# Kernel tuning notes

Hardware: AMD Instinct MI355X
Metric: run time of the kernel (lower is better)

Reference implementation:

```python
import jax, jax.numpy as jnp
import numpy as np

N_NODES = 50000
N_EDGES = 800000
D_IN = 128
D_HID = 128
D_OUT = 128


def setup_inputs() -> dict:
    key = jax.random.key(0)
    ks = jax.random.split(key, 10)
    x = jax.random.normal(ks[0], (N_NODES, D_IN), dtype=jnp.float32)
    edge_index = jax.random.randint(ks[1], (2, N_EDGES), 0, N_NODES, dtype=jnp.int64)
    edge_index_inter = jax.random.randint(ks[2], (2, N_EDGES), 0, N_NODES, dtype=jnp.int64)
    # nn.Linear-style params: W [out, in], b [out]
    def linear(k, fan_in, fan_out):
        k1, k2 = jax.random.split(k)
        bound = 1.0 / np.sqrt(fan_in)
        W = jax.random.uniform(k1, (fan_out, fan_in), minval=-bound, maxval=bound, dtype=jnp.float32)
        b = jax.random.uniform(k2, (fan_out,), minval=-bound, maxval=bound, dtype=jnp.float32)
        return W, b
    W1, b1 = linear(ks[3], D_IN, D_HID)
    W2, b2 = linear(ks[4], D_HID, D_HID)
    W3, b3 = linear(ks[5], D_HID, D_OUT)
    return {"x": x, "W1": W1, "b1": b1, "W2": W2, "b2": b2, "W3": W3, "b3": b3,
            "edge_index": edge_index, "edge_index_inter": edge_index_inter}


def _gnn_layer(h, W, b, src, dst, n_nodes):
    # message: lin(x_j - x_i); x_j = source features, x_i = target features (PyG convention)
    msg = (h[src] - h[dst]) @ W.T + b          # [E, out]
    # aggr='add': scatter-add messages into target nodes
    return jax.ops.segment_sum(msg, dst, num_segments=n_nodes)  # [N, out]


def reference(x, W1, b1, W2, b2, W3, b3, edge_index, edge_index_inter):
    src, dst = edge_index[0], edge_index[1]
    n = x.shape[0]
    h = _gnn_layer(x, W1, b1, src, dst, n)
    h = _gnn_layer(h, W2, b2, src, dst, n)
    return _gnn_layer(h, W3, b3, src, dst, n)
```

## Files before the change

### kernel.cpp

```cpp
#include <hip/hip_runtime.h>

#define N_NODES 50000
#define N_EDGES 800000
#define D 128
#define TN 16
#define TSTR 136
#define SCAN_BLOCKS 196

typedef __attribute__((ext_vector_type(8))) short bf16x8;
typedef __attribute__((ext_vector_type(4))) float f32x4;

__device__ __forceinline__ unsigned short f32_to_bf16_rne(float f) {
    unsigned u = __float_as_uint(f);
    u += 0x7fffu + ((u >> 16) & 1u);
    return (unsigned short)(u >> 16);
}

__global__ void prep_kernel(const int* __restrict__ dst, int* __restrict__ counts,
                            const float* __restrict__ x, unsigned short* __restrict__ xb) {
    const int t = blockIdx.x * blockDim.x + threadIdx.x;
    if (t < N_EDGES) atomicAdd(&counts[dst[t]], 1);
    {
        const float4 v0 = *(const float4*)(x + (size_t)t * 8);
        const float4 v1 = *(const float4*)(x + (size_t)t * 8 + 4);
        uint4 p;
        p.x = (unsigned)f32_to_bf16_rne(v0.x) | ((unsigned)f32_to_bf16_rne(v0.y) << 16);
        p.y = (unsigned)f32_to_bf16_rne(v0.z) | ((unsigned)f32_to_bf16_rne(v0.w) << 16);
        p.z = (unsigned)f32_to_bf16_rne(v1.x) | ((unsigned)f32_to_bf16_rne(v1.y) << 16);
        p.w = (unsigned)f32_to_bf16_rne(v1.z) | ((unsigned)f32_to_bf16_rne(v1.w) << 16);
        *(uint4*)(xb + (size_t)t * 8) = p;
    }
}

__global__ void block_sum_kernel(const int* __restrict__ counts, int* __restrict__ bsum) {
    __shared__ int red[256];
    const int tid = threadIdx.x;
    const int i = blockIdx.x * 256 + tid;
    red[tid] = (i < N_NODES) ? counts[i] : 0;
    __syncthreads();
    for (int s = 128; s > 0; s >>= 1) {
        if (tid < s) red[tid] += red[tid + s];
        __syncthreads();
    }
    if (tid == 0) bsum[blockIdx.x] = red[0];
}

__global__ void bsum_scan_kernel(const int* __restrict__ bsum,
                                 int* __restrict__ bpre,
                                 int* __restrict__ offsets) {
    __shared__ int s[256];
    const int tid = threadIdx.x;
    const int v = (tid < SCAN_BLOCKS) ? bsum[tid] : 0;
    s[tid] = v;
    __syncthreads();
    for (int off = 1; off < 256; off <<= 1) {
        int a = (tid >= off) ? s[tid - off] : 0;
        __syncthreads();
        s[tid] += a;
        __syncthreads();
    }
    bpre[tid] = s[tid] - v;
    if (tid == 255) offsets[N_NODES] = s[255];
}

__global__ void offsets_wfrag_kernel(const int* __restrict__ counts,
                                     const int* __restrict__ bpre,
                                     int* __restrict__ offsets,
                                     int* __restrict__ cursor,
                                     const float* __restrict__ W1,
                                     const float* __restrict__ W2,
                                     const float* __restrict__ W3,
                                     unsigned short* __restrict__ Wb) {
    if (blockIdx.x < SCAN_BLOCKS) {
        __shared__ int s[256];
        const int tid = threadIdx.x;
        const int i = blockIdx.x * 256 + tid;
        const int v = (i < N_NODES) ? counts[i] : 0;
        s[tid] = v;
        __syncthreads();
        for (int off = 1; off < 256; off <<= 1) {
            int a = (tid >= off) ? s[tid - off] : 0;
            __syncthreads();
            s[tid] += a;
            __syncthreads();
        }
        const int excl = s[tid] - v + bpre[blockIdx.x];
        if (i < N_NODES) {
            offsets[i] = excl;
            cursor[i] = excl;
        }
    } else {
        const int unit = (blockIdx.x - SCAN_BLOCKS) * 2 + (threadIdx.x >> 7);
        const int w = unit >> 7;
        const int o = unit & 127;
        const int k = threadIdx.x & 127;
        const float* W = (w == 0) ? W1 : (w == 1) ? W2 : W3;
        const unsigned short v = f32_to_bf16_rne(W[o * D + k]);
        const int nt = o >> 4, n = o & 15;
        const int kc = k >> 5, kr = k & 31, quad = kr >> 3, j = kr & 7;
        const int lane = quad * 16 + n;
        Wb[(((size_t)w * 8 + nt) * 4 + kc) * 512 + lane * 8 + j] = v;
    }
}

__global__ void fill_kernel(const int* __restrict__ src, const int* __restrict__ dst,
                            int* __restrict__ cursor, int* __restrict__ esrc) {
    int e = blockIdx.x * blockDim.x + threadIdx.x;
    if (e < N_EDGES) {
        int v = dst[e];
        int p = atomicAdd(&cursor[v], 1);
        esrc[p] = src[e];
    }
}

template <bool OUT_BF16>
__global__ __launch_bounds__(256) void gnn_layer_kernel(
    const unsigned short* __restrict__ hb,
    const int* __restrict__ offsets,
    const int* __restrict__ esrc,
    const unsigned short* __restrict__ Wb,
    const float* __restrict__ bias,
    float* __restrict__ outf,
    unsigned short* __restrict__ outb) {

    __shared__ __align__(16) unsigned short tb[TN][TSTR];
    __shared__ float degf[TN];

    const int tid = threadIdx.x;
    const int wave = tid >> 6;
    const int lane = tid & 63;
    const int sub = lane >> 5;
    const int q = lane & 31;
    const int vbase = blockIdx.x * TN;

    for (int j = wave * 4; j < wave * 4 + 4; ++j) {
        const int v = vbase + j;
        const int beg = offsets[v];
        const int end = offsets[v + 1];
        const int deg = end - beg;

        float a0x = 0.f, a0y = 0.f, a0z = 0.f, a0w = 0.f;
        float a1x = 0.f, a1y = 0.f, a1z = 0.f, a1w = 0.f;
        float a2x = 0.f, a2y = 0.f, a2z = 0.f, a2w = 0.f;
        float a3x = 0.f, a3y = 0.f, a3z = 0.f, a3w = 0.f;

        if (deg <= 64) {
            int myidx = 0;
            if (lane < deg) myidx = esrc[beg + lane];

            int i = 0;
            for (; i + 8 <= deg; i += 8) {
                const int s0 = __shfl(myidx, i + sub, 64);
                const int s1 = __shfl(myidx, i + 2 + sub, 64);
                const int s2 = __shfl(myidx, i + 4 + sub, 64);
                const int s3 = __shfl(myidx, i + 6 + sub, 64);
                const uint2 r0 = *(const uint2*)(hb + (size_t)s0 * D + 4 * q);
                const uint2 r1 = *(const uint2*)(hb + (size_t)s1 * D + 4 * q);
                const uint2 r2 = *(const uint2*)(hb + (size_t)s2 * D + 4 * q);
                const uint2 r3 = *(const uint2*)(hb + (size_t)s3 * D + 4 * q);
                a0x += __uint_as_float(r0.x << 16); a0y += __uint_as_float(r0.x & 0xffff0000u);
                a0z += __uint_as_float(r0.y << 16); a0w += __uint_as_float(r0.y & 0xffff0000u);
                a1x += __uint_as_float(r1.x << 16); a1y += __uint_as_float(r1.x & 0xffff0000u);
                a1z += __uint_as_float(r1.y << 16); a1w += __uint_as_float(r1.y & 0xffff0000u);
                a2x += __uint_as_float(r2.x << 16); a2y += __uint_as_float(r2.x & 0xffff0000u);
                a2z += __uint_as_float(r2.y << 16); a2w += __uint_as_float(r2.y & 0xffff0000u);
                a3x += __uint_as_float(r3.x << 16); a3y += __uint_as_float(r3.x & 0xffff0000u);
                a3z += __uint_as_float(r3.y << 16); a3w += __uint_as_float(r3.y & 0xffff0000u);
            }
            for (; i + 2 <= deg; i += 2) {
                const int s0 = __shfl(myidx, i + sub, 64);
                const uint2 r0 = *(const uint2*)(hb + (size_t)s0 * D + 4 * q);
                a0x += __uint_as_float(r0.x << 16); a0y += __uint_as_float(r0.x & 0xffff0000u);
                a0z += __uint_as_float(r0.y << 16); a0w += __uint_as_float(r0.y & 0xffff0000u);
            }
            if (i < deg) {
                const int s0 = __shfl(myidx, i, 64);
                if (sub == 0) {
                    const uint2 r0 = *(const uint2*)(hb + (size_t)s0 * D + 4 * q);
                    a0x += __uint_as_float(r0.x << 16); a0y += __uint_as_float(r0.x & 0xffff0000u);
                    a0z += __uint_as_float(r0.y << 16); a0w += __uint_as_float(r0.y & 0xffff0000u);
                }
            }
        } else {
            for (int e = beg; e < end; e += 2) {
                const int e0 = e + sub;
                if (e0 < end) {
                    const uint2 r0 = *(const uint2*)(hb + (size_t)esrc[e0] * D + 4 * q);
                    a0x += __uint_as_float(r0.x << 16); a0y += __uint_as_float(r0.x & 0xffff0000u);
                    a0z += __uint_as_float(r0.y << 16); a0w += __uint_as_float(r0.y & 0xffff0000u);
                }
            }
        }

        float ax = (a0x + a1x) + (a2x + a3x);
        float ay = (a0y + a1y) + (a2y + a3y);
        float az = (a0z + a1z) + (a2z + a3z);
        float aw = (a0w + a1w) + (a2w + a3w);

        ax += __shfl_xor(ax, 32, 64);
        ay += __shfl_xor(ay, 32, 64);
        az += __shfl_xor(az, 32, 64);
        aw += __shfl_xor(aw, 32, 64);

        const float dv = (float)deg;
        if (sub == 0) {
            const uint2 r = *(const uint2*)(hb + (size_t)v * D + 4 * q);
            const float tx = ax - dv * __uint_as_float(r.x << 16);
            const float ty = ay - dv * __uint_as_float(r.x & 0xffff0000u);
            const float tz = az - dv * __uint_as_float(r.y << 16);
            const float tw = aw - dv * __uint_as_float(r.y & 0xffff0000u);
            unsigned p0 = (unsigned)f32_to_bf16_rne(tx) | ((unsigned)f32_to_bf16_rne(ty) << 16);
            unsigned p1 = (unsigned)f32_to_bf16_rne(tz) | ((unsigned)f32_to_bf16_rne(tw) << 16);
            *(uint2*)&tb[j][4 * q] = make_uint2(p0, p1);
        }
        if (lane == 0) degf[j] = dv;
    }
    __syncthreads();

    const int n16 = lane & 15;
    const int quad = lane >> 4;

    bf16x8 afrag[4];
#pragma unroll
    for (int kc = 0; kc < 4; ++kc)
        afrag[kc] = *(const bf16x8*)&tb[n16][kc * 32 + quad * 8];

#pragma unroll
    for (int i = 0; i < 2; ++i) {
        const int nt = wave * 2 + i;
        f32x4 acc = {0.f, 0.f, 0.f, 0.f};
#pragma unroll
        for (int kc = 0; kc < 4; ++kc) {
            const bf16x8 bfrag = *(const bf16x8*)&Wb[((nt * 4 + kc) * 64 + lane) * 8];
            acc = __builtin_amdgcn_mfma_f32_16x16x32_bf16(afrag[kc], bfrag, acc, 0, 0, 0);
        }
        const int o = nt * 16 + n16;
        const float bo = bias[o];
#pragma unroll
        for (int r = 0; r < 4; ++r) {
            const int m = quad * 4 + r;
            const float val = acc[r] + degf[m] * bo;
            if (OUT_BF16)
                outb[(size_t)(vbase + m) * D + o] = f32_to_bf16_rne(val);
            else
                outf[(size_t)(vbase + m) * D + o] = val;
        }
    }
}

extern "C" void kernel_launch(void* const* d_in, const int* in_sizes, int n_in,
                              void* d_out, int out_size, void* d_ws, size_t ws_size,
                              hipStream_t stream) {
    const float* x  = (const float*)d_in[0];
    const float* W1 = (const float*)d_in[1];
    const float* b1 = (const float*)d_in[2];
    const float* W2 = (const float*)d_in[3];
    const float* b2 = (const float*)d_in[4];
    const float* W3 = (const float*)d_in[5];
    const float* b3 = (const float*)d_in[6];
    const int*   ei = (const int*)d_in[7];

    const int* src = ei;
    const int* dst = ei + N_EDGES;
    float* out = (float*)d_out;

    char* ws = (char*)d_ws;
    int* counts  = (int*)ws;                      ws += 204800;
    int* offsets = (int*)ws;                      ws += 204800;
    int* cursor  = (int*)ws;                      ws += 204800;
    int* bsum    = (int*)ws;                      ws += 1024;
    int* bpre    = (int*)ws;                      ws += 1024;
    int* esrc    = (int*)ws;                      ws += (size_t)N_EDGES * 4;
    unsigned short* Wb = (unsigned short*)ws;     ws += 3 * 16384 * 2;
    unsigned short* xb = (unsigned short*)ws;     ws += (size_t)N_NODES * D * 2;
    unsigned short* h1 = (unsigned short*)ws;     ws += (size_t)N_NODES * D * 2;
    unsigned short* h2 = (unsigned short*)ws;

    hipMemsetAsync(counts, 0, N_NODES * sizeof(int), stream);
    prep_kernel<<<(N_EDGES + 255) / 256, 256, 0, stream>>>(dst, counts, x, xb);
    block_sum_kernel<<<SCAN_BLOCKS, 256, 0, stream>>>(counts, bsum);
    bsum_scan_kernel<<<1, 256, 0, stream>>>(bsum, bpre, offsets);
    offsets_wfrag_kernel<<<SCAN_BLOCKS + 192, 256, 0, stream>>>(counts, bpre, offsets, cursor,
                                                                W1, W2, W3, Wb);
    fill_kernel<<<(N_EDGES + 255) / 256, 256, 0, stream>>>(src, dst, cursor, esrc);

    const int blocks = N_NODES / TN;

    gnn_layer_kernel<true ><<<blocks, 256, 0, stream>>>(xb, offsets, esrc, Wb,          b1, nullptr, h1);
    gnn_layer_kernel<true ><<<blocks, 256, 0, stream>>>(h1, offsets, esrc, Wb + 16384,  b2, nullptr, h2);
    gnn_layer_kernel<false><<<blocks, 256, 0, stream>>>(h2, offsets, esrc, Wb + 32768,  b3, out, nullptr);
}
```

Before: 289.4 us.

## Split fused gather+GEMM into separate column-sliced gather and MFMA GEMM kernels

Splits each layer's fused aggregate-then-MFMA kernel into two kernels. The first is a gather that splits the 128 features into four 32-column slices, one per block group, with a wave per node and 8 edges processed in parallel per pass. The second is a small GEMM kernel that reads the aggregated bf16 rows from a global buffer. CSR construction also records per-edge atomic ranks during counting, which removes the second atomic cursor pass in fill. The cost is an extra global round-trip of the aggregated tensor and more kernel launches, in exchange for finer-grained gather parallelism and a possibly better cache footprint per feature slice.

```diff
diff --git a/kernel.cpp b/kernel.cpp
--- a/kernel.cpp
+++ b/kernel.cpp
@@ -3,7 +3,6 @@
 #define N_NODES 50000
 #define N_EDGES 800000
 #define D 128
-#define TN 16
 #define TSTR 136
 #define SCAN_BLOCKS 196
 
@@ -16,10 +15,20 @@
     return (unsigned short)(u >> 16);
 }
 
+__device__ __forceinline__ void acc_bf16x4(uint2 r, float& x, float& y, float& z, float& w) {
+    x += __uint_as_float(r.x << 16);
+    y += __uint_as_float(r.x & 0xffff0000u);
+    z += __uint_as_float(r.y << 16);
+    w += __uint_as_float(r.y & 0xffff0000u);
+}
+
 __global__ void prep_kernel(const int* __restrict__ dst, int* __restrict__ counts,
+                            int* __restrict__ rank,
                             const float* __restrict__ x, unsigned short* __restrict__ xb) {
     const int t = blockIdx.x * blockDim.x + threadIdx.x;
-    if (t < N_EDGES) atomicAdd(&counts[dst[t]], 1);
+    if (t < N_EDGES) {
+        rank[t] = atomicAdd(&counts[dst[t]], 1);
+    }
     {
         const float4 v0 = *(const float4*)(x + (size_t)t * 8);
         const float4 v1 = *(const float4*)(x + (size_t)t * 8 + 4);
@@ -66,7 +75,6 @@
 __global__ void offsets_wfrag_kernel(const int* __restrict__ counts,
                                      const int* __restrict__ bpre,
                                      int* __restrict__ offsets,
-                                     int* __restrict__ cursor,
                                      const float* __restrict__ W1,
                                      const float* __restrict__ W2,
                                      const float* __restrict__ W3,
@@ -85,10 +93,7 @@
             __syncthreads();
         }
         const int excl = s[tid] - v + bpre[blockIdx.x];
-        if (i < N_NODES) {
-            offsets[i] = excl;
-            cursor[i] = excl;
-        }
+        if (i < N_NODES) offsets[i] = excl;
     } else {
         const int unit = (blockIdx.x - SCAN_BLOCKS) * 2 + (threadIdx.x >> 7);
         const int w = unit >> 7;
@@ -104,119 +109,104 @@
 }
 
 __global__ void fill_kernel(const int* __restrict__ src, const int* __restrict__ dst,
-                            int* __restrict__ cursor, int* __restrict__ esrc) {
+                            const int* __restrict__ rank,
+                            const int* __restrict__ offsets, int* __restrict__ esrc) {
     int e = blockIdx.x * blockDim.x + threadIdx.x;
     if (e < N_EDGES) {
-        int v = dst[e];
-        int p = atomicAdd(&cursor[v], 1);
-        esrc[p] = src[e];
-    }
-}
-
-template <bool OUT_BF16>
-__global__ __launch_bounds__(256) void gnn_layer_kernel(
+        esrc[offsets[dst[e]] + rank[e]] = src[e];
+    }
+}
+
+__global__ __launch_bounds__(256) void gather_kernel(
     const unsigned short* __restrict__ hb,
     const int* __restrict__ offsets,
     const int* __restrict__ esrc,
+    unsigned short* __restrict__ tg) {
+
+    const int bid = blockIdx.x;
+    const int ky = (bid & 7) >> 1;
+    const int ng = ((bid >> 3) << 1) + (bid & 1);
+    const int wave = threadIdx.x >> 6;
+    const int lane = threadIdx.x & 63;
+    const int g = lane >> 3;
+    const int d = lane & 7;
+    const int v = ng * 4 + wave;
+    const int col = ky * 32 + d * 4;
+
+    const int beg = offsets[v];
+    const int deg = offsets[v + 1] - beg;
+
+    float ax = 0.f, ay = 0.f, az = 0.f, aw = 0.f;
+    float bx = 0.f, by = 0.f, bz = 0.f, bw = 0.f;
+
+    for (int base = 0; base < deg; base += 64) {
+        const int cnt = min(deg - base, 64);
+        int myidx = 0;
+        if (lane < cnt) myidx = esrc[beg + base + lane];
+
+        for (int i = 0; i < cnt; i += 16) {
+            const int e0 = i + g;
+            const int e1 = i + 8 + g;
+            const int s0 = __shfl(myidx, e0, 64);
+            const int s1 = __shfl(myidx, e1, 64);
+            if (e0 < cnt) {
+                const uint2 r = *(const uint2*)(hb + (size_t)s0 * D + col);
+                acc_bf16x4(r, ax, ay, az, aw);
+            }
+            if (e1 < cnt) {
+                const uint2 r = *(const uint2*)(hb + (size_t)s1 * D + col);
+                acc_bf16x4(r, bx, by, bz, bw);
+            }
+        }
+    }
+    ax += bx; ay += by; az += bz; aw += bw;
+
+#pragma unroll
+    for (int m = 8; m <= 32; m <<= 1) {
+        ax += __shfl_xor(ax, m, 64);
+        ay += __shfl_xor(ay, m, 64);
+        az += __shfl_xor(az, m, 64);
+        aw += __shfl_xor(aw, m, 64);
+    }
+
+    if (g == 0) {
+        const float dv = (float)deg;
+        const uint2 r = *(const uint2*)(hb + (size_t)v * D + col);
+        const float tx = ax - dv * __uint_as_float(r.x << 16);
+        const float ty = ay - dv * __uint_as_float(r.x & 0xffff0000u);
+        const float tz = az - dv * __uint_as_float(r.y << 16);
+        const float tw = aw - dv * __uint_as_float(r.y & 0xffff0000u);
+        unsigned p0 = (unsigned)f32_to_bf16_rne(tx) | ((unsigned)f32_to_bf16_rne(ty) << 16);
+        unsigned p1 = (unsigned)f32_to_bf16_rne(tz) | ((unsigned)f32_to_bf16_rne(tw) << 16);
+        *(uint2*)(tg + (size_t)v * D + col) = make_uint2(p0, p1);
+    }
+}
+
+template <bool OUT_BF16>
+__global__ __launch_bounds__(256) void gemm_kernel(
+    const unsigned short* __restrict__ tg,
+    const int* __restrict__ offsets,
     const unsigned short* __restrict__ Wb,
     const float* __restrict__ bias,
     float* __restrict__ outf,
     unsigned short* __restrict__ outb) {
 
-    __shared__ __align__(16) unsigned short tb[TN][TSTR];
-    __shared__ float degf[TN];
+    __shared__ __align__(16) unsigned short tb[16][TSTR];
+    __shared__ float degf[16];
 
     const int tid = threadIdx.x;
+    const int vbase = blockIdx.x * 16;
+
+    {
+        const int row = tid >> 4;
+        const int c8 = (tid & 15) * 8;
+        *(uint4*)&tb[row][c8] = *(const uint4*)(tg + (size_t)(vbase + row) * D + c8);
+    }
+    if (tid < 16) degf[tid] = (float)(offsets[vbase + tid + 1] - offsets[vbase + tid]);
+    __syncthreads();
+
     const int wave = tid >> 6;
     const int lane = tid & 63;
-    const int sub = lane >> 5;
-    const int q = lane & 31;
-    const int vbase = blockIdx.x * TN;
-
-    for (int j = wave * 4; j < wave * 4 + 4; ++j) {
-        const int v = vbase + j;
-        const int beg = offsets[v];
-        const int end = offsets[v + 1];
-        const int deg = end - beg;
-
-        float a0x = 0.f, a0y = 0.f, a0z = 0.f, a0w = 0.f;
-        float a1x = 0.f, a1y = 0.f, a1z = 0.f, a1w = 0.f;
-        float a2x = 0.f, a2y = 0.f, a2z = 0.f, a2w = 0.f;
-        float a3x = 0.f, a3y = 0.f, a3z = 0.f, a3w = 0.f;
-
-        if (deg <= 64) {
-            int myidx = 0;
-            if (lane < deg) myidx = esrc[beg + lane];
-
-            int i = 0;
-            for (; i + 8 <= deg; i += 8) {
-                const int s0 = __shfl(myidx, i + sub, 64);
-                const int s1 = __shfl(myidx, i + 2 + sub, 64);
-                const int s2 = __shfl(myidx, i + 4 + sub, 64);
-                const int s3 = __shfl(myidx, i + 6 + sub, 64);
-                const uint2 r0 = *(const uint2*)(hb + (size_t)s0 * D + 4 * q);
-                const uint2 r1 = *(const uint2*)(hb + (size_t)s1 * D + 4 * q);
-                const uint2 r2 = *(const uint2*)(hb + (size_t)s2 * D + 4 * q);
-                const uint2 r3 = *(const uint2*)(hb + (size_t)s3 * D + 4 * q);
-                a0x += __uint_as_float(r0.x << 16); a0y += __uint_as_float(r0.x & 0xffff0000u);
-                a0z += __uint_as_float(r0.y << 16); a0w += __uint_as_float(r0.y & 0xffff0000u);
-                a1x += __uint_as_float(r1.x << 16); a1y += __uint_as_float(r1.x & 0xffff0000u);
-                a1z += __uint_as_float(r1.y << 16); a1w += __uint_as_float(r1.y & 0xffff0000u);
-                a2x += __uint_as_float(r2.x << 16); a2y += __uint_as_float(r2.x & 0xffff0000u);
-                a2z += __uint_as_float(r2.y << 16); a2w += __uint_as_float(r2.y & 0xffff0000u);
-                a3x += __uint_as_float(r3.x << 16); a3y += __uint_as_float(r3.x & 0xffff0000u);
-                a3z += __uint_as_float(r3.y << 16); a3w += __uint_as_float(r3.y & 0xffff0000u);
-            }
-            for (; i + 2 <= deg; i += 2) {
-                const int s0 = __shfl(myidx, i + sub, 64);
-                const uint2 r0 = *(const uint2*)(hb + (size_t)s0 * D + 4 * q);
-                a0x += __uint_as_float(r0.x << 16); a0y += __uint_as_float(r0.x & 0xffff0000u);
-                a0z += __uint_as_float(r0.y << 16); a0w += __uint_as_float(r0.y & 0xffff0000u);
-            }
-            if (i < deg) {
-                const int s0 = __shfl(myidx, i, 64);
-                if (sub == 0) {
-                    const uint2 r0 = *(const uint2*)(hb + (size_t)s0 * D + 4 * q);
-                    a0x += __uint_as_float(r0.x << 16); a0y += __uint_as_float(r0.x & 0xffff0000u);
-                    a0z += __uint_as_float(r0.y << 16); a0w += __uint_as_float(r0.y & 0xffff0000u);
-                }
-            }
-        } else {
-            for (int e = beg; e < end; e += 2) {
-                const int e0 = e + sub;
-                if (e0 < end) {
-                    const uint2 r0 = *(const uint2*)(hb + (size_t)esrc[e0] * D + 4 * q);
-                    a0x += __uint_as_float(r0.x << 16); a0y += __uint_as_float(r0.x & 0xffff0000u);
-                    a0z += __uint_as_float(r0.y << 16); a0w += __uint_as_float(r0.y & 0xffff0000u);
-                }
-            }
-        }
-
-        float ax = (a0x + a1x) + (a2x + a3x);
-        float ay = (a0y + a1y) + (a2y + a3y);
-        float az = (a0z + a1z) + (a2z + a3z);
-        float aw = (a0w + a1w) + (a2w + a3w);
-
-        ax += __shfl_xor(ax, 32, 64);
-        ay += __shfl_xor(ay, 32, 64);
-        az += __shfl_xor(az, 32, 64);
-        aw += __shfl_xor(aw, 32, 64);
-
-        const float dv = (float)deg;
-        if (sub == 0) {
-            const uint2 r = *(const uint2*)(hb + (size_t)v * D + 4 * q);
-            const float tx = ax - dv * __uint_as_float(r.x << 16);
-            const float ty = ay - dv * __uint_as_float(r.x & 0xffff0000u);
-            const float tz = az - dv * __uint_as_float(r.y << 16);
-            const float tw = aw - dv * __uint_as_float(r.y & 0xffff0000u);
-            unsigned p0 = (unsigned)f32_to_bf16_rne(tx) | ((unsigned)f32_to_bf16_rne(ty) << 16);
-            unsigned p1 = (unsigned)f32_to_bf16_rne(tz) | ((unsigned)f32_to_bf16_rne(tw) << 16);
-            *(uint2*)&tb[j][4 * q] = make_uint2(p0, p1);
-        }
-        if (lane == 0) degf[j] = dv;
-    }
-    __syncthreads();
-
     const int n16 = lane & 15;
     const int quad = lane >> 4;
 
@@ -267,26 +257,31 @@
     char* ws = (char*)d_ws;
     int* counts  = (int*)ws;                      ws += 204800;
     int* offsets = (int*)ws;                      ws += 204800;
-    int* cursor  = (int*)ws;                      ws += 204800;
     int* bsum    = (int*)ws;                      ws += 1024;
     int* bpre    = (int*)ws;                      ws += 1024;
+    int* rank    = (int*)ws;                      ws += (size_t)N_EDGES * 4;
     int* esrc    = (int*)ws;                      ws += (size_t)N_EDGES * 4;
     unsigned short* Wb = (unsigned short*)ws;     ws += 3 * 16384 * 2;
     unsigned short* xb = (unsigned short*)ws;     ws += (size_t)N_NODES * D * 2;
     unsigned short* h1 = (unsigned short*)ws;     ws += (size_t)N_NODES * D * 2;
-    unsigned short* h2 = (unsigned short*)ws;
+    unsigned short* h2 = (unsigned short*)ws;     ws += (size_t)N_NODES * D * 2;
+    unsigned short* tg = (unsigned short*)ws;     ws += (size_t)N_NODES * D * 2;
 
     hipMemsetAsync(counts, 0, N_NODES * sizeof(int), stream);
-    prep_kernel<<<(N_EDGES + 255) / 256, 256, 0, stream>>>(dst, counts, x, xb);
+    prep_kernel<<<(N_EDGES + 255) / 256, 256, 0, stream>>>(dst, counts, rank, x, xb);
     block_sum_kernel<<<SCAN_BLOCKS, 256, 0, stream>>>(counts, bsum);
     bsum_scan_kernel<<<1, 256, 0, stream>>>(bsum, bpre, offsets);
-    offsets_wfrag_kernel<<<SCAN_BLOCKS + 192, 256, 0, stream>>>(counts, bpre, offsets, cursor,
+    offsets_wfrag_kernel<<<SCAN_BLOCKS + 192, 256, 0, stream>>>(counts, bpre, offsets,
                                                                 W1, W2, W3, Wb);
-    fill_kernel<<<(N_EDGES + 255) / 256, 256, 0, stream>>>(src, dst, cursor, esrc);
-
-    const int blocks = N_NODES / TN;
-
-    gnn_layer_kernel<true ><<<blocks, 256, 0, stream>>>(xb, offsets, esrc, Wb,          b1, nullptr, h1);
-    gnn_layer_kernel<true ><<<blocks, 256, 0, stream>>>(h1, offsets, esrc, Wb + 16384,  b2, nullptr, h2);
-    gnn_layer_kernel<false><<<blocks, 256, 0, stream>>>(h2, offsets, esrc, Wb + 32768,  b3, out, nullptr);
-}
+    fill_kernel<<<(N_EDGES + 255) / 256, 256, 0, stream>>>(src, dst, rank, offsets, esrc);
+
+    const int gblocks = (N_NODES / 4) * 4;
+    const int mblocks = N_NODES / 16;
+
+    gather_kernel<<<gblocks, 256, 0, stream>>>(xb, offsets, esrc, tg);
+    gemm_kernel<true ><<<mblocks, 256, 0, stream>>>(tg, offsets, Wb,         b1, nullptr, h1);
+    gather_kernel<<<gblocks, 256, 0, stream>>>(h1, offsets, esrc, tg);
+    gemm_kernel<true ><<<mblocks, 256, 0, stream>>>(tg, offsets, Wb + 16384, b2, nullptr, h2);
+    gather_kernel<<<gblocks, 256, 0, stream>>>(h2, offsets, esrc, tg);
+    gemm_kernel<false><<<mblocks, 256, 0, stream>>>(tg, offsets, Wb + 32768, b3, out, nullptr);
+}
```

After: 392.5 us. 35.6% more time.
